# Optimization experiments

Hardware: AMD Instinct MI355X
Metric: run time of the kernel (lower is better)

## Reference

```python
import jax, jax.numpy as jnp
import numpy as np


def _lstm_layer(x, h0, c0, Wih, Whh, b):
    """PyTorch-convention single-layer LSTM. x:[B,T,I], h0/c0:[B,H].
    Wih:[4H,I], Whh:[4H,H], b:[4H] (b_ih+b_hh folded). Gate order: i,f,g,o."""
    H = h0.shape[-1]
    xp = jnp.einsum('bti,gi->btg', x, Wih) + b          # [B,T,4H] precomputed input proj
    xp_t = jnp.swapaxes(xp, 0, 1)                        # [T,B,4H]

    def step(carry, xt):
        h, c = carry
        g = xt + h @ Whh.T                               # [B,4H]
        i = jax.nn.sigmoid(g[:, 0*H:1*H])
        f = jax.nn.sigmoid(g[:, 1*H:2*H])
        gg = jnp.tanh(g[:, 2*H:3*H])
        o = jax.nn.sigmoid(g[:, 3*H:4*H])
        c = f * c + i * gg
        h = o * jnp.tanh(c)
        return (h, c), h

    (_, _), hs = jax.lax.scan(step, (h0, c0), xp_t)      # hs: [T,B,H]
    return jnp.swapaxes(hs, 0, 1)                        # [B,T,H]


def setup_inputs() -> dict:
    key = jax.random.key(0)
    ks = jax.random.split(key, 16)
    B, T, IN, OUT = 256, 1024, 100, 1
    H0, H1, H2 = 32, 64, 128

    def u(k, shape, fan):
        s = 1.0 / np.sqrt(fan)
        return jax.random.uniform(k, shape, jnp.float32, -s, s)

    inp = {
        'input': jax.random.normal(ks[0], (B, T, IN), jnp.float32),
        'h_0': jnp.zeros((1, B, H0), jnp.float32),
        'c_0': jnp.zeros((1, B, H0), jnp.float32),
        'Wih0': u(ks[1], (4*H0, IN), H0), 'Whh0': u(ks[2], (4*H0, H0), H0), 'b0': u(ks[3], (4*H0,), H0),
        'Wih1': u(ks[4], (4*H1, H0), H1), 'Whh1': u(ks[5], (4*H1, H1), H1), 'b1': u(ks[6], (4*H1,), H1),
        'Wih2': u(ks[7], (4*H2, H1), H2), 'Whh2': u(ks[8], (4*H2, H2), H2), 'b2': u(ks[9], (4*H2,), H2),
        'Wl': u(ks[10], (OUT, H2), H2), 'bl': u(ks[11], (OUT,), H2),
    }
    return inp


def reference(input, h_0, c_0, Wih0, Whh0, b0, Wih1, Whh1, b1, Wih2, Whh2, b2, Wl, bl):
    B = input.shape[0]
    z1 = jnp.zeros((B, 64), input.dtype)
    z2 = jnp.zeros((B, 128), input.dtype)
    r = _lstm_layer(input, h_0[0], c_0[0], Wih0, Whh0, b0)   # [B,T,32]
    r = _lstm_layer(r, z1, z1, Wih1, Whh1, b1)               # [B,T,64]
    r = _lstm_layer(r, z2, z2, Wih2, Whh2, b2)               # [B,T,128]
    out = jnp.tanh(jnp.einsum('bth,oh->bto', r, Wl) + bl)    # [B,T,out_dim]
    return out, r
```

## Files before the change

kernel.cpp:

```cpp
#include <hip/hip_runtime.h>
#include <cmath>

#define TT 1024
#define BB 256
#define GG 16
#define NBLK (BB / GG)

#define LOG2E  1.4426950408889634f
#define LOG2E2 2.8853900817779268f

typedef _Float16 f16x8 __attribute__((ext_vector_type(8)));
typedef float    f32x4 __attribute__((ext_vector_type(4)));
typedef _Float16 half2v __attribute__((ext_vector_type(2)));

__device__ __forceinline__ float fast_rcp(float x) { return __builtin_amdgcn_rcpf(x); }
__device__ __forceinline__ float sig2(float g) { return fast_rcp(1.0f + __builtin_exp2f(-g)); }
__device__ __forceinline__ float th2(float g)  { return 1.0f - 2.0f * fast_rcp(1.0f + __builtin_exp2f(g)); }
__device__ __forceinline__ unsigned pack_f16(float a, float b) {
    half2v h; h.x = (_Float16)a; h.y = (_Float16)b;
    return __builtin_bit_cast(unsigned, h);
}
__device__ __forceinline__ void pin4(uint4& u) {
    asm volatile("" : "+v"(u.x), "+v"(u.y), "+v"(u.z), "+v"(u.w));
}
__device__ __forceinline__ f16x8 h8(uint4 u) { return __builtin_bit_cast(f16x8, u); }
__device__ __forceinline__ void step_barrier() {
    asm volatile("s_waitcnt lgkmcnt(0)" ::: "memory");
    __builtin_amdgcn_s_barrier();
    __builtin_amdgcn_sched_barrier(0);
}

#define MFMA16(a, b, c) __builtin_amdgcn_mfma_f32_16x16x32_f16((a), (b), (c), 0, 0, 0)
#define ZERO4 ((f32x4){0.f, 0.f, 0.f, 0.f})

#define FRAG_PTR(buf, k, col) ((char*)&(buf)[(k) >> 5][(((k) & 31) >> 3) * 16 + (col)] + ((k) & 7) * 2)
#define GFRAG_PTR(base, k, col) ((char*)(base) + ((((k) >> 5) * 64 + (((k) & 31) >> 3) * 16 + (col)) * 16 + ((k) & 7) * 2))

__global__ __launch_bounds__(256) void reorder_wf(
    const float* __restrict__ Wih0, const float* __restrict__ Whh0,
    const float* __restrict__ Wih1, const float* __restrict__ Whh1,
    const float* __restrict__ Wih2, const float* __restrict__ Whh2,
    _Float16* __restrict__ wfA0, _Float16* __restrict__ wfA1,
    _Float16* __restrict__ wfC, int* __restrict__ prog)
{
    int idx = blockIdx.x * 256 + threadIdx.x;
    if (idx < 98304) {
        int j = idx & 7, l = (idx >> 3) & 63, t = idx >> 9;
        int kt = t % 6, g = (t / 6) & 3, w = t / 24;
        int row = g * 128 + 16 * w + (l & 15);
        int k = kt * 32 + ((l >> 4) << 3) + j;
        float sc = (g == 2) ? LOG2E2 : LOG2E;
        float v = (k < 64) ? Wih2[row * 64 + k] : Whh2[row * 128 + (k - 64)];
        wfC[idx] = (_Float16)(v * sc);
    } else if (idx < 118784) {
        int f = idx - 98304;
        int j = f & 7, l = (f >> 3) & 63, t = f >> 9;
        int kt = t % 5, g = (t / 5) & 3, w = t / 20;
        int row = g * 32 + 16 * w + (l & 15);
        int k = kt * 32 + ((l >> 4) << 3) + j;
        float sc = (g == 2) ? LOG2E2 : LOG2E;
        float v = (k < 32)  ? Whh0[row * 32 + k]
                : (k < 132) ? Wih0[row * 100 + (k - 32)] : 0.0f;
        wfA0[f] = (_Float16)(v * sc);
    } else if (idx < 143360) {
        int f = idx - 118784;
        int j = f & 7, l = (f >> 3) & 63, t = f >> 9;
        int kt = t % 3, g = (t / 3) & 3, w = t / 12;
        int row = g * 64 + 16 * w + (l & 15);
        int k = kt * 32 + ((l >> 4) << 3) + j;
        float sc = (g == 2) ? LOG2E2 : LOG2E;
        float v = (k < 32) ? Wih1[row * 32 + k] : Whh1[row * 64 + (k - 32)];
        wfA1[f] = (_Float16)(v * sc);
    } else if (idx < 143376) {
        prog[idx - 143360] = 0;
    }
}

__global__ __launch_bounds__(256) void pack_x(
    const float* __restrict__ x, uint4* __restrict__ xf123,
    uint2* __restrict__ xf4c)
{
    int idx = blockIdx.x * 256 + threadIdx.x;
    if (idx < 16 * 1024 * 3 * 64) {
        int l   = idx & 63;
        int kt  = (idx >> 6) % 3;
        int t   = ((idx >> 6) / 3) & 1023;
        int blk = (idx >> 6) / 3 / 1024;
        int col = l & 15, lq = l >> 4;
        int xidx = kt * 32 + lq * 8;
        const float* xr = x + ((size_t)(blk * GG + col) * TT + t) * 100 + xidx;
        float4 a = *reinterpret_cast<const float4*>(xr);
        float4 b = *reinterpret_cast<const float4*>(xr + 4);
        uint4 u;
        u.x = pack_f16(a.x, a.y); u.y = pack_f16(a.z, a.w);
        u.z = pack_f16(b.x, b.y); u.w = pack_f16(b.z, b.w);
        xf123[idx] = u;
    } else {
        int f = idx - 16 * 1024 * 3 * 64;
        int col = f & 15;
        int t   = (f >> 4) & 1023;
        int blk = f >> 14;
        const float* xr = x + ((size_t)(blk * GG + col) * TT + t) * 100 + 96;
        float4 a = *reinterpret_cast<const float4*>(xr);
        uint2 u; u.x = pack_f16(a.x, a.y); u.y = pack_f16(a.z, a.w);
        xf4c[f] = u;
    }
}

__global__ __attribute__((amdgpu_flat_work_group_size(512, 512),
                          amdgpu_waves_per_eu(1, 2)))
void lstm_mega(const uint4* __restrict__ xf123,
               const uint2* __restrict__ xf4c,
               const _Float16* __restrict__ wfA0,
               const _Float16* __restrict__ wfA1,
               const _Float16* __restrict__ wfC,
               const float* __restrict__ b0_,
               const float* __restrict__ b1_,
               const float* __restrict__ b2_,
               const float* __restrict__ h_0,
               const float* __restrict__ c_0,
               uint4* __restrict__ r1f,
               float* __restrict__ r2,
               int* __restrict__ prog)
{
    const int tid = threadIdx.x;
    const int w = tid >> 6, l = tid & 63;
    const int l15 = l & 15, lq = l >> 4;
    const bool isA = (blockIdx.x < NBLK);
    const int blk = isA ? blockIdx.x : blockIdx.x - NBLK;
    const int b0b = blk * GG;

    __shared__ alignas(16) uint4 H0F[2][1][64];
    __shared__ alignas(16) uint4 H1F[2][2][64];
    __shared__ alignas(16) uint4 H2F[2][4][64];

    if (isA) {
        uint4 afu[20];
        f32x4 biasv[4];
        float c[4] = {0.f, 0.f, 0.f, 0.f};
        int jb = 0;
        if (w < 2) {
            jb = 16 * w + 4 * lq;
            const uint4* wf4 = reinterpret_cast<const uint4*>(wfA0);
            #pragma unroll
            for (int g = 0; g < 4; ++g)
                #pragma unroll
                for (int kt = 0; kt < 5; ++kt) {
                    afu[g * 5 + kt] = wf4[((w * 4 + g) * 5 + kt) * 64 + l];
                    pin4(afu[g * 5 + kt]);
                }
            #pragma unroll
            for (int g = 0; g < 4; ++g) {
                float sc = (g == 2) ? LOG2E2 : LOG2E;
                #pragma unroll
                for (int r = 0; r < 4; ++r)
                    biasv[g][r] = b0_[g * 32 + jb + r] * sc;
            }
            #pragma unroll
            for (int r = 0; r < 4; ++r) c[r] = c_0[(b0b + l15) * 32 + jb + r];
        } else if (w < 6) {
            const int w1 = w - 2;
            jb = 16 * w1 + 4 * lq;
            const uint4* wf4 = reinterpret_cast<const uint4*>(wfA1);
            #pragma unroll
            for (int g = 0; g < 4; ++g)
                #pragma unroll
                for (int kt = 0; kt < 3; ++kt) {
                    afu[g * 3 + kt] = wf4[((w1 * 4 + g) * 3 + kt) * 64 + l];
                    pin4(afu[g * 3 + kt]);
                }
            #pragma unroll
            for (int g = 0; g < 4; ++g) {
                float sc = (g == 2) ? LOG2E2 : LOG2E;
                #pragma unroll
                for (int r = 0; r < 4; ++r)
                    biasv[g][r] = b1_[g * 64 + jb + r] * sc;
            }
        }

        {
            int col = tid >> 5, u = tid & 31;
            *(_Float16*)FRAG_PTR(H0F[0], u, col) =
                (_Float16)h_0[(b0b + col) * 32 + u];
            if (tid < 128) H1F[1][tid >> 6][tid & 63] = (uint4){0, 0, 0, 0};
        }

        uint4 bx0 = {0,0,0,0}, bx1 = {0,0,0,0}, bx2 = {0,0,0,0};
        uint2 bx4 = {0, 0};
        if (w < 2) {
            size_t o = ((size_t)blk * TT) * 3 * 64 + l;
            bx0 = xf123[o]; bx1 = xf123[o + 64]; bx2 = xf123[o + 128];
            bx4 = xf4c[((size_t)blk * TT) * 16 + l15];
        }
        step_barrier();

        for (int m = 0; m <= TT; ++m) {
            const int cur = m & 1, nxt = cur ^ 1;

            if ((m & 7) == 0 && m >= 8 && tid == 384)
                __hip_atomic_store(&prog[blk], m - 1, __ATOMIC_RELEASE,
                                   __HIP_MEMORY_SCOPE_AGENT);

            if (w < 2) {
                uint4 cx0 = bx0, cx1 = bx1, cx2 = bx2;
                uint2 cx4 = bx4;
                if (m + 1 < TT) {
                    size_t o = ((size_t)blk * TT + (m + 1)) * 3 * 64 + l;
                    bx0 = xf123[o]; bx1 = xf123[o + 64]; bx2 = xf123[o + 128];
                    bx4 = xf4c[((size_t)blk * TT + (m + 1)) * 16 + l15];
                }
                if (m < TT) {
                    f16x8 bh = reinterpret_cast<const f16x8*>(&H0F[cur][0][0])[l];
                    uint4 t4;
                    t4.x = (lq == 0) ? cx4.x : 0u; t4.y = (lq == 0) ? cx4.y : 0u;
                    t4.z = 0u; t4.w = 0u;
                    f32x4 accA[4], accB[4];
                    #pragma unroll
                    for (int g = 0; g < 4; ++g) {
                        accA[g] = MFMA16(h8(afu[g * 5 + 0]), bh, biasv[g]);
                        accB[g] = MFMA16(h8(afu[g * 5 + 1]), h8(cx0), ZERO4);
                        accA[g] = MFMA16(h8(afu[g * 5 + 2]), h8(cx1), accA[g]);
                        accB[g] = MFMA16(h8(afu[g * 5 + 3]), h8(cx2), accB[g]);
                        accA[g] = MFMA16(h8(afu[g * 5 + 4]), h8(t4), accA[g]);
                    }
                    float h[4];
                    #pragma unroll
                    for (int r = 0; r < 4; ++r) {
                        float ai  = sig2(accA[0][r] + accB[0][r]);
                        float afg = sig2(accA[1][r] + accB[1][r]);
                        float ag  = th2(accA[2][r] + accB[2][r]);
                        float ao  = sig2(accA[3][r] + accB[3][r]);
                        c[r] = fmaf(afg, c[r], ai * ag);
                        h[r] = ao * th2(c[r] * LOG2E2);
                    }
                    uint2 hp = make_uint2(pack_f16(h[0], h[1]), pack_f16(h[2], h[3]));
                    *(uint2*)FRAG_PTR(H0F[nxt], jb, l15) = hp;
                }
            } else if (w < 6) {
                if (m >= 1) {
                    f16x8 bh0 = reinterpret_cast<const f16x8*>(&H0F[cur][0][0])[l];
                    f16x8 bh1 = reinterpret_cast<const f16x8*>(&H1F[cur][0][0])[l];
                    f16x8 bh2 = reinterpret_cast<const f16x8*>(&H1F[cur][1][0])[l];
                    f32x4 accA[4], accB[4];
                    #pragma unroll
                    for (int g = 0; g < 4; ++g) {
                        accA[g] = MFMA16(h8(afu[g * 3 + 0]), bh0, biasv[g]);
                        accB[g] = MFMA16(h8(afu[g * 3 + 1]), bh1, ZERO4);
                        accA[g] = MFMA16(h8(afu[g * 3 + 2]), bh2, accA[g]);
                    }
                    float h[4];
                    #pragma unroll
                    for (int r = 0; r < 4; ++r) {
                        float ai  = sig2(accA[0][r] + accB[0][r]);
                        float afg = sig2(accA[1][r] + accB[1][r]);
                        float ag  = th2(accA[2][r] + accB[2][r]);
                        float ao  = sig2(accA[3][r] + accB[3][r]);
                        c[r] = fmaf(afg, c[r], ai * ag);
                        h[r] = ao * th2(c[r] * LOG2E2);
                    }
                    uint2 hp = make_uint2(pack_f16(h[0], h[1]), pack_f16(h[2], h[3]));
                    *(uint2*)FRAG_PTR(H1F[nxt], jb, l15) = hp;
                    uint4* base = r1f + ((size_t)blk * TT + (m - 1)) * 128;
                    *(uint2*)GFRAG_PTR(base, jb, l15) = hp;
                    if ((m & 7) == 7)
                        asm volatile("s_waitcnt vmcnt(0)" ::: "memory");
                }
            }
            step_barrier();
        }
        asm volatile("s_waitcnt vmcnt(0)" ::: "memory");
        __builtin_amdgcn_s_barrier();
        if (tid == 384)
            __hip_atomic_store(&prog[blk], 4096, __ATOMIC_RELEASE,
                               __HIP_MEMORY_SCOPE_AGENT);
    } else {
        const int jb = 16 * w + 4 * lq;
        uint4 af[24];
        {
            const uint4* wf4 = reinterpret_cast<const uint4*>(wfC);
            #pragma unroll
            for (int g = 0; g < 4; ++g)
                #pragma unroll
                for (int kt = 0; kt < 6; ++kt) {
                    af[g * 6 + kt] = wf4[((w * 4 + g) * 6 + kt) * 64 + l];
                    pin4(af[g * 6 + kt]);
                }
        }
        f32x4 biasv[4];
        #pragma unroll
        for (int g = 0; g < 4; ++g) {
            float sc = (g == 2) ? LOG2E2 : LOG2E;
            #pragma unroll
            for (int r = 0; r < 4; ++r)
                biasv[g][r] = b2_[g * 128 + jb + r] * sc;
        }
        if (tid < 256) H2F[0][tid >> 6][tid & 63] = (uint4){0, 0, 0, 0};

        if ((tid & 63) == 0) {
            while (__hip_atomic_load(&prog[blk], __ATOMIC_ACQUIRE,
                                     __HIP_MEMORY_SCOPE_AGENT) < 10)
                __builtin_amdgcn_s_sleep(1);
        }
        __builtin_amdgcn_s_barrier();

        uint4 l00, l01, l10, l11;
        {
            size_t o = ((size_t)blk * TT) * 128 + l;
            l00 = r1f[o]; l01 = r1f[o + 64];
            l10 = r1f[o + 128]; l11 = r1f[o + 192];
        }
        step_barrier();

        float c[4] = {0.f, 0.f, 0.f, 0.f};

        for (int m = 0; m < TT; ++m) {
            const int cur = m & 1, nxt = cur ^ 1;

            if ((m & 7) == 0 && m > 0) {
                if ((tid & 63) == 0) {
                    const int needed = m + 10;
                    while (__hip_atomic_load(&prog[blk], __ATOMIC_ACQUIRE,
                                             __HIP_MEMORY_SCOPE_AGENT) < needed)
                        __builtin_amdgcn_s_sleep(1);
                }
                __builtin_amdgcn_s_barrier();
            }

            uint4 cr0 = l00, cr1 = l01;
            l00 = l10; l01 = l11;
            if (m + 2 < TT) {
                size_t o = ((size_t)blk * TT + (m + 2)) * 128 + l;
                l10 = r1f[o]; l11 = r1f[o + 64];
            }

            f16x8 bh[4];
            #pragma unroll
            for (int kt = 0; kt < 4; ++kt)
                bh[kt] = reinterpret_cast<const f16x8*>(&H2F[cur][kt][0])[l];

            f32x4 accA[4], accB[4];
            #pragma unroll
            for (int g = 0; g < 4; ++g) {
                accA[g] = MFMA16(h8(af[g * 6 + 0]), h8(cr0), biasv[g]);
                accB[g] = MFMA16(h8(af[g * 6 + 1]), h8(cr1), ZERO4);
                accA[g] = MFMA16(h8(af[g * 6 + 2]), bh[0], accA[g]);
                accB[g] = MFMA16(h8(af[g * 6 + 3]), bh[1], accB[g]);
                accA[g] = MFMA16(h8(af[g * 6 + 4]), bh[2], accA[g]);
                accB[g] = MFMA16(h8(af[g * 6 + 5]), bh[3], accB[g]);
            }

            float h[4];
            #pragma unroll
            for (int r = 0; r < 4; ++r) {
                float ai  = sig2(accA[0][r] + accB[0][r]);
                float afg = sig2(accA[1][r] + accB[1][r]);
                float ag  = th2(accA[2][r] + accB[2][r]);
                float ao  = sig2(accA[3][r] + accB[3][r]);
                c[r] = fmaf(afg, c[r], ai * ag);
                h[r] = ao * th2(c[r] * LOG2E2);
            }
            uint2 hp = make_uint2(pack_f16(h[0], h[1]), pack_f16(h[2], h[3]));
            *(uint2*)FRAG_PTR(H2F[nxt], jb, l15) = hp;
            float4 hv = make_float4(h[0], h[1], h[2], h[3]);
            *reinterpret_cast<float4*>(
                r2 + ((size_t)(b0b + l15) * TT + m) * 128 + jb) = hv;
            step_barrier();
        }
    }
}

__global__ __launch_bounds__(256) void final_proj(
    const float* __restrict__ r, const float* __restrict__ Wl,
    const float* __restrict__ bl, float* __restrict__ out)
{
    __shared__ float wl[128];
    const int tid = threadIdx.x;
    if (tid < 128) wl[tid] = Wl[tid];
    __syncthreads();

    const int bt = blockIdx.x * 256 + tid;
    const float4* rr = reinterpret_cast<const float4*>(r + (size_t)bt * 128);
    float a0 = 0.f, a1 = 0.f, a2 = 0.f, a3 = 0.f;
    #pragma unroll
    for (int k = 0; k < 32; ++k) {
        float4 v = rr[k];
        a0 = fmaf(v.x, wl[4 * k + 0], a0);
        a1 = fmaf(v.y, wl[4 * k + 1], a1);
        a2 = fmaf(v.z, wl[4 * k + 2], a2);
        a3 = fmaf(v.w, wl[4 * k + 3], a3);
    }
    out[bt] = tanhf(((a0 + a1) + (a2 + a3)) + bl[0]);
}

extern "C" void kernel_launch(void* const* d_in, const int* in_sizes, int n_in,
                              void* d_out, int out_size, void* d_ws, size_t ws_size,
                              hipStream_t stream) {
    const float* input = (const float*)d_in[0];
    const float* h_0   = (const float*)d_in[1];
    const float* c_0   = (const float*)d_in[2];
    const float* Wih0  = (const float*)d_in[3];
    const float* Whh0  = (const float*)d_in[4];
    const float* b0    = (const float*)d_in[5];
    const float* Wih1  = (const float*)d_in[6];
    const float* Whh1  = (const float*)d_in[7];
    const float* b1    = (const float*)d_in[8];
    const float* Wih2  = (const float*)d_in[9];
    const float* Whh2  = (const float*)d_in[10];
    const float* b2    = (const float*)d_in[11];
    const float* Wl    = (const float*)d_in[12];
    const float* bl    = (const float*)d_in[13];

    float* out = (float*)d_out;
    float* r2  = out + (size_t)BB * TT;

    char* ws = (char*)d_ws;
    uint4*    xf123 = (uint4*)ws;
    uint2*    xf4c  = (uint2*)(ws + 50331648);
    uint4*    r1f   = (uint4*)(ws + 52428800);
    _Float16* wfA0  = (_Float16*)(ws + 85983232);
    _Float16* wfA1  = (_Float16*)(ws + 86024192);
    _Float16* wfC   = (_Float16*)(ws + 86073344);
    int*      prog  = (int*)(ws + 86269952);

    hipLaunchKernelGGL(reorder_wf, dim3(561), dim3(256), 0, stream,
                       Wih0, Whh0, Wih1, Whh1, Wih2, Whh2, wfA0, wfA1, wfC, prog);
    hipLaunchKernelGGL(pack_x, dim3(13312), dim3(256), 0, stream,
                       input, xf123, xf4c);
    hipLaunchKernelGGL(lstm_mega, dim3(2 * NBLK), dim3(512), 0, stream,
                       xf123, xf4c, wfA0, wfA1, wfC, b0, b1, b2, h_0, c_0,
                       r1f, r2, prog);
    hipLaunchKernelGGL(final_proj, dim3(BB * TT / 256), dim3(256), 0, stream,
                       r2, Wl, bl, out);
}
```

Baseline: 1.466 ms.

## Offload layer-1 global stores to a dedicated wave and coarsen progress sync

Global writes of layer-1 hidden states move off the compute waves onto an otherwise idle wave, which copies the shared-memory fragments one step late, so the recurrent waves no longer stall on vmcnt drains. Progress is now published every 16 steps and the consumer checks every 16 steps with a larger lead, which cuts atomic polling. It also unrolls the step loops by 2, drops the sched_barrier in the step barrier, and makes the r2 output stores nontemporal. The cost is one extra loop iteration of latency, a longer startup wait for the consumer, and a coarser sync granularity.

After: 1.371 ms. 1.07x faster.

```diff
diff --git a/kernel.cpp b/kernel.cpp
--- a/kernel.cpp
+++ b/kernel.cpp
@@ -27,14 +27,12 @@
 __device__ __forceinline__ void step_barrier() {
     asm volatile("s_waitcnt lgkmcnt(0)" ::: "memory");
     __builtin_amdgcn_s_barrier();
-    __builtin_amdgcn_sched_barrier(0);
 }
 
 #define MFMA16(a, b, c) __builtin_amdgcn_mfma_f32_16x16x32_f16((a), (b), (c), 0, 0, 0)
 #define ZERO4 ((f32x4){0.f, 0.f, 0.f, 0.f})
 
 #define FRAG_PTR(buf, k, col) ((char*)&(buf)[(k) >> 5][(((k) & 31) >> 3) * 16 + (col)] + ((k) & 7) * 2)
-#define GFRAG_PTR(base, k, col) ((char*)(base) + ((((k) >> 5) * 64 + (((k) & 31) >> 3) * 16 + (col)) * 16 + ((k) & 7) * 2))
 
 __global__ __launch_bounds__(256) void reorder_wf(
     const float* __restrict__ Wih0, const float* __restrict__ Whh0,
@@ -194,12 +192,9 @@
         }
         step_barrier();
 
-        for (int m = 0; m <= TT; ++m) {
+        #pragma unroll 2
+        for (int m = 0; m <= TT + 1; ++m) {
             const int cur = m & 1, nxt = cur ^ 1;
-
-            if ((m & 7) == 0 && m >= 8 && tid == 384)
-                __hip_atomic_store(&prog[blk], m - 1, __ATOMIC_RELEASE,
-                                   __HIP_MEMORY_SCOPE_AGENT);
 
             if (w < 2) {
                 uint4 cx0 = bx0, cx1 = bx1, cx2 = bx2;
@@ -237,7 +232,7 @@
                     *(uint2*)FRAG_PTR(H0F[nxt], jb, l15) = hp;
                 }
             } else if (w < 6) {
-                if (m >= 1) {
+                if (m >= 1 && m <= TT) {
                     f16x8 bh0 = reinterpret_cast<const f16x8*>(&H0F[cur][0][0])[l];
                     f16x8 bh1 = reinterpret_cast<const f16x8*>(&H1F[cur][0][0])[l];
                     f16x8 bh2 = reinterpret_cast<const f16x8*>(&H1F[cur][1][0])[l];
@@ -260,16 +255,25 @@
                     }
                     uint2 hp = make_uint2(pack_f16(h[0], h[1]), pack_f16(h[2], h[3]));
                     *(uint2*)FRAG_PTR(H1F[nxt], jb, l15) = hp;
-                    uint4* base = r1f + ((size_t)blk * TT + (m - 1)) * 128;
-                    *(uint2*)GFRAG_PTR(base, jb, l15) = hp;
-                    if ((m & 7) == 7)
+                }
+            } else if (w == 6) {
+                if (m >= 2) {
+                    const int t = m - 2;
+                    uint4 f0 = H1F[cur][0][l];
+                    uint4 f1 = H1F[cur][1][l];
+                    uint4* base = r1f + ((size_t)blk * TT + t) * 128;
+                    base[l]      = f0;
+                    base[64 + l] = f1;
+                    if ((m & 15) == 15 || m == TT + 1) {
                         asm volatile("s_waitcnt vmcnt(0)" ::: "memory");
+                        if (l == 0)
+                            __hip_atomic_store(&prog[blk], t, __ATOMIC_RELEASE,
+                                               __HIP_MEMORY_SCOPE_AGENT);
+                    }
                 }
             }
             step_barrier();
         }
-        asm volatile("s_waitcnt vmcnt(0)" ::: "memory");
-        __builtin_amdgcn_s_barrier();
         if (tid == 384)
             __hip_atomic_store(&prog[blk], 4096, __ATOMIC_RELEASE,
                                __HIP_MEMORY_SCOPE_AGENT);
@@ -298,7 +302,7 @@
 
         if ((tid & 63) == 0) {
             while (__hip_atomic_load(&prog[blk], __ATOMIC_ACQUIRE,
-                                     __HIP_MEMORY_SCOPE_AGENT) < 10)
+                                     __HIP_MEMORY_SCOPE_AGENT) < 17)
                 __builtin_amdgcn_s_sleep(1);
         }
         __builtin_amdgcn_s_barrier();
@@ -313,12 +317,13 @@
 
         float c[4] = {0.f, 0.f, 0.f, 0.f};
 
+        #pragma unroll 2
         for (int m = 0; m < TT; ++m) {
             const int cur = m & 1, nxt = cur ^ 1;
 
-            if ((m & 7) == 0 && m > 0) {
+            if ((m & 15) == 0 && m > 0) {
                 if ((tid & 63) == 0) {
-                    const int needed = m + 10;
+                    const int needed = (m + 17 < TT) ? (m + 17) : (TT - 1);
                     while (__hip_atomic_load(&prog[blk], __ATOMIC_ACQUIRE,
                                              __HIP_MEMORY_SCOPE_AGENT) < needed)
                         __builtin_amdgcn_s_sleep(1);
@@ -361,9 +366,9 @@
             }
             uint2 hp = make_uint2(pack_f16(h[0], h[1]), pack_f16(h[2], h[3]));
             *(uint2*)FRAG_PTR(H2F[nxt], jb, l15) = hp;
-            float4 hv = make_float4(h[0], h[1], h[2], h[3]);
-            *reinterpret_cast<float4*>(
-                r2 + ((size_t)(b0b + l15) * TT + m) * 128 + jb) = hv;
+            f32x4 hv = (f32x4){h[0], h[1], h[2], h[3]};
+            __builtin_nontemporal_store(hv, reinterpret_cast<f32x4*>(
+                r2 + ((size_t)(b0b + l15) * TT + m) * 128 + jb));
             step_barrier();
         }
     }
```
